# Performance work log

Measured on AMD Instinct MI355X. Metric: run time of the kernel, lower is better.

## Reference

```python
import jax, jax.numpy as jnp
from jax import lax
import numpy as np

R = 256            # reservoir_size
LUT_LEN = 18       # 2**18 LUT entries per node
B = 8              # bits_per_feature
D = 4              # n_features
M = 512            # samples
S = 512            # steps
OUT = 10           # output_size


def _first_primes(n):
    sieve = np.ones(2000, dtype=bool)
    sieve[:2] = False
    for i in range(2, 45):
        if sieve[i]:
            sieve[i * i::i] = False
    return np.nonzero(sieve)[0][:n].astype(np.int32)


def setup_inputs() -> dict:
    key = jax.random.key(0)
    ks = jax.random.split(key, 7)
    x = jax.random.randint(ks[0], (M, S, D, B), 0, 2).astype(bool)
    lut = jax.random.randint(ks[1], (R, 2 ** LUT_LEN), 0, 2).astype(jnp.int32)
    init_res = jax.random.randint(ks[2], (R,), 0, 2).astype(bool)
    W_res = jax.random.randint(ks[3], (R, R), 0, 2).astype(bool)
    input_nodes = jax.random.permutation(ks[4], R)[: B * D].astype(jnp.int32)
    primes = jnp.asarray(_first_primes(R))
    readout_W = jax.random.normal(ks[5], (OUT, R), dtype=jnp.float32) * (1.0 / np.sqrt(R))
    readout_b = jax.random.normal(ks[6], (OUT,), dtype=jnp.float32) * 0.01
    return {
        "x": x,
        "input_nodes": input_nodes,
        "lut": lut,
        "W_res": W_res,
        "primes": primes,
        "init_res": init_res,
        "readout_W": readout_W,
        "readout_b": readout_b,
    }


def _run_reservoir(x, input_nodes, lut, W_res, primes, init_res):
    m, s, d, b = x.shape
    xf = x.reshape(m, s, d * b).astype(jnp.int32)          # [m, s, d*b]
    # row j of Wp holds primes[k] * W_res[j, k]; idx = r @ Wp.T
    Wp = W_res.astype(jnp.int32) * primes[None, :]          # [R, R]
    node_idx = jnp.arange(R)[None, :]                       # [1, R]
    r0 = jnp.broadcast_to(init_res.astype(jnp.int32), (m, R))

    def step(r, x_t):
        # write encoded input bits into the reservoir, then LUT-perturb
        r = r.at[:, input_nodes].set(x_t)                   # [m, R]
        idx = r @ Wp.T                                      # [m, R] state indices
        r_new = jnp.take_along_axis(lut[None].repeat(1, 0)[0][node_idx.repeat(m, 0) * 0 + node_idx, idx], jnp.zeros((m, R, 1), jnp.int32), axis=-1) if False else lut[node_idx, idx]
        return r_new.astype(jnp.int32), None

    rf, _ = lax.scan(step, r0, jnp.swapaxes(xf, 0, 1))      # scan over s steps
    return rf                                               # [m, R] final states (0/1)


def reference(x, input_nodes, lut, W_res, primes, init_res, readout_W, readout_b):
    rf = _run_reservoir(x, input_nodes, lut, W_res, primes, init_res)
    return rf.astype(jnp.float32) @ readout_W.T + readout_b  # [m, output_size]
```

## Files before the change

### kernel.cpp

```cpp
#include <hip/hip_runtime.h>
#include <stdint.h>

#define R_NODES 256
#define M_SAMP  512
#define S_STEPS 512
#define OUT_N   10

__global__ void detect_layout(const uint8_t* __restrict__ x, int* __restrict__ flag) {
    __shared__ int any;
    if (threadIdx.x == 0) any = 0;
    __syncthreads();
    int acc = 0;
    for (int i = 0; i < 64; ++i)
        acc |= x[(size_t)(threadIdx.x * 64 + i) * 4 + 1];
    if (acc) atomicOr(&any, 1);
    __syncthreads();
    if (threadIdx.x == 0) *flag = any ? 1 : 0;
}

__global__ void pack_x(const uint8_t* __restrict__ x, const int* __restrict__ flag,
                       uint32_t* __restrict__ xp) {
    const int stride = (*flag) ? 1 : 4;
    const int f = blockIdx.x * blockDim.x + threadIdx.x;
    const int val = x[(size_t)f * stride];
    const uint64_t mask = __ballot(val != 0);
    const int lane = threadIdx.x & 63;
    if ((lane & 31) == 0) {
        uint32_t w = (lane & 32) ? (uint32_t)(mask >> 32) : (uint32_t)mask;
        xp[f >> 5] = w;
    }
}

__device__ __forceinline__ uint32_t spread8(uint32_t x) {
    x = (x | (x << 12)) & 0x000F000Fu;
    x = (x | (x << 6))  & 0x03030303u;
    x = (x | (x << 3))  & 0x11111111u;
    return x;
}
__global__ void pack_lut(const int* __restrict__ lut, uint32_t* __restrict__ lp32) {
    const int lane = threadIdx.x & 63;
    const int gw = blockIdx.x * (blockDim.x >> 6) + (threadIdx.x >> 6);
    const int4* src = (const int4*)lut;
    for (int it = 0; it < 16; ++it) {
        const int chunk = gw * 16 + it;
        const int4 q = src[(size_t)chunk * 64 + lane];
        const uint64_t b0 = __ballot((q.x & 1) != 0);
        const uint64_t b1 = __ballot((q.y & 1) != 0);
        const uint64_t b2 = __ballot((q.z & 1) != 0);
        const uint64_t b3 = __ballot((q.w & 1) != 0);
        if (lane < 8) {
            const uint32_t B0 = (uint32_t)(b0 >> (8 * lane)) & 0xFF;
            const uint32_t B1 = (uint32_t)(b1 >> (8 * lane)) & 0xFF;
            const uint32_t B2 = (uint32_t)(b2 >> (8 * lane)) & 0xFF;
            const uint32_t B3 = (uint32_t)(b3 >> (8 * lane)) & 0xFF;
            const uint32_t w = spread8(B0) | (spread8(B1) << 1)
                             | (spread8(B2) << 2) | (spread8(B3) << 3);
            lp32[(size_t)chunk * 8 + lane] = w;
        }
    }
}

__global__ __launch_bounds__(256, 2) void reservoir_pop(
    const uint32_t* __restrict__ xp, const uint64_t* __restrict__ lp,
    const int* __restrict__ input_nodes, const uint8_t* __restrict__ wres,
    const int* __restrict__ primes, const uint8_t* __restrict__ init_res,
    const int* __restrict__ flag, const float* __restrict__ rW,
    const float* __restrict__ rb, float* __restrict__ out)
{
    const int m = blockIdx.x;
    const int j = threadIdx.x;
    const int l = j & 63;
    const int w = j >> 6;
    const int stride = (*flag) ? 1 : 4;

    __shared__ uint32_t sxw[S_STEPS];
    __shared__ uint32_t rmask[2][8];
    __shared__ float    lout[OUT_N];

    const uint32_t* xrow = xp + m * S_STEPS;
    for (int i = j; i < S_STEPS; i += 256) sxw[i] = xrow[i];

    int slot = -1;
    for (int i = 0; i < 32; ++i)
        if (input_nodes[i] == j) slot = i;

    uint32_t PW[11][8];
#pragma unroll
    for (int b = 0; b < 11; ++b)
#pragma unroll
        for (int q = 0; q < 8; ++q) PW[b][q] = 0;
#pragma unroll
    for (int q = 0; q < 8; ++q) {
        for (int bit = 0; bit < 32; ++bit) {
            const int k = 32 * q + bit;
            const uint32_t on = wres[(size_t)(j * 256 + k) * stride] ? 1u : 0u;
            const uint32_t p  = on * (uint32_t)primes[k];
#pragma unroll
            for (int b = 0; b < 11; ++b)
                PW[b][q] |= ((p >> b) & 1u) << bit;
        }
    }

    __syncthreads();
    {
        int bv = init_res[(size_t)j * stride] ? 1 : 0;
        if (slot >= 0) bv = (sxw[0] >> slot) & 1;
        const uint64_t bal = __ballot(bv != 0);
        if (l == 0) {
            rmask[0][2 * w]     = (uint32_t)bal;
            rmask[0][2 * w + 1] = (uint32_t)(bal >> 32);
        }
    }
    __syncthreads();

    int cur = 0;
    int v = 0;
    for (int s = 0; s < S_STEPS; ++s) {
        const uint32_t R0 = rmask[cur][0], R1 = rmask[cur][1],
                       R2 = rmask[cur][2], R3 = rmask[cur][3],
                       R4 = rmask[cur][4], R5 = rmask[cur][5],
                       R6 = rmask[cur][6], R7 = rmask[cur][7];
        uint32_t idx = 0;
#pragma unroll
        for (int b = 0; b < 11; ++b) {
            uint32_t a;
            a  = (uint32_t)__popc(PW[b][0] & R0);
            a += (uint32_t)__popc(PW[b][1] & R1);
            a += (uint32_t)__popc(PW[b][2] & R2);
            a += (uint32_t)__popc(PW[b][3] & R3);
            a += (uint32_t)__popc(PW[b][4] & R4);
            a += (uint32_t)__popc(PW[b][5] & R5);
            a += (uint32_t)__popc(PW[b][6] & R6);
            a += (uint32_t)__popc(PW[b][7] & R7);
            idx += a << b;
        }

        const uint64_t wv = lp[((size_t)j << 12) + (idx >> 6)];
        v = (int)((wv >> (idx & 63)) & 1);

        int wb = v;
        if (s + 1 < S_STEPS && slot >= 0) wb = (sxw[s + 1] >> slot) & 1;
        const uint64_t bal = __ballot(wb != 0);
        if (l == 0) {
            rmask[cur ^ 1][2 * w]     = (uint32_t)bal;
            rmask[cur ^ 1][2 * w + 1] = (uint32_t)(bal >> 32);
        }
        __syncthreads();
        cur ^= 1;
    }

    if (j < OUT_N) lout[j] = 0.f;
    __syncthreads();
#pragma unroll
    for (int o = 0; o < OUT_N; ++o) {
        float c = v ? rW[o * R_NODES + j] : 0.f;
        for (int off = 32; off > 0; off >>= 1)
            c += __shfl_down(c, off, 64);
        if (l == 0) atomicAdd(&lout[o], c);
    }
    __syncthreads();
    if (j < OUT_N) out[m * OUT_N + j] = lout[j] + rb[j];
}

extern "C" void kernel_launch(void* const* d_in, const int* in_sizes, int n_in,
                              void* d_out, int out_size, void* d_ws, size_t ws_size,
                              hipStream_t stream) {
    const uint8_t* x        = (const uint8_t*)d_in[0];
    const int* input_nodes  = (const int*)d_in[1];
    const int* lut          = (const int*)d_in[2];
    const uint8_t* wres     = (const uint8_t*)d_in[3];
    const int* primes       = (const int*)d_in[4];
    const uint8_t* init_res = (const uint8_t*)d_in[5];
    const float* rW         = (const float*)d_in[6];
    const float* rb         = (const float*)d_in[7];
    float* out              = (float*)d_out;

    uint8_t* ws = (uint8_t*)d_ws;
    int*      flag = (int*)ws;
    uint32_t* xp   = (uint32_t*)(ws + 4096);
    uint64_t* lp   = (uint64_t*)(ws + 4096 + 1048576);

    detect_layout<<<1, 256, 0, stream>>>(x, flag);
    pack_x<<<(M_SAMP * S_STEPS * 32) / 256, 256, 0, stream>>>(x, flag, xp);
    pack_lut<<<4096, 256, 0, stream>>>(lut, (uint32_t*)lp);
    reservoir_pop<<<M_SAMP, 256, 0, stream>>>(xp, lp, input_nodes, wres,
                                              primes, init_res, flag,
                                              rW, rb, out);
}
```

Baseline: 1.061 ms.

## Process two samples per block to overlap LUT gathers and share per-node weights

Each block now runs two samples' reservoirs together. This reuses the per-thread packed prime-weight registers and halves the number of barriers per sample-step. The LUT lookup for sample B is issued while sample A's index is still being computed, using inline-asm global loads and explicit vmcnt waits, so the two memory latencies overlap inside one wave. The cost is that the grid shrinks to 256 blocks with launch bounds of one block per SIMD set, which lowers occupancy and relies on hand-scheduled asm waits.

```diff
diff --git a/kernel.cpp b/kernel.cpp
--- a/kernel.cpp
+++ b/kernel.cpp
@@ -5,6 +5,8 @@
 #define M_SAMP  512
 #define S_STEPS 512
 #define OUT_N   10
+
+typedef unsigned int u32x2 __attribute__((ext_vector_type(2)));
 
 __global__ void detect_layout(const uint8_t* __restrict__ x, int* __restrict__ flag) {
     __shared__ int any;
@@ -60,25 +62,26 @@
     }
 }
 
-__global__ __launch_bounds__(256, 2) void reservoir_pop(
+__global__ __launch_bounds__(256, 1) void reservoir_pop2(
     const uint32_t* __restrict__ xp, const uint64_t* __restrict__ lp,
     const int* __restrict__ input_nodes, const uint8_t* __restrict__ wres,
     const int* __restrict__ primes, const uint8_t* __restrict__ init_res,
     const int* __restrict__ flag, const float* __restrict__ rW,
     const float* __restrict__ rb, float* __restrict__ out)
 {
-    const int m = blockIdx.x;
+    const int m2 = blockIdx.x;
     const int j = threadIdx.x;
     const int l = j & 63;
     const int w = j >> 6;
     const int stride = (*flag) ? 1 : 4;
 
-    __shared__ uint32_t sxw[S_STEPS];
-    __shared__ uint32_t rmask[2][8];
-    __shared__ float    lout[OUT_N];
-
-    const uint32_t* xrow = xp + m * S_STEPS;
-    for (int i = j; i < S_STEPS; i += 256) sxw[i] = xrow[i];
+    __shared__ uint32_t sxwA[S_STEPS], sxwB[S_STEPS];
+    __shared__ uint32_t rmask[2][2][8];
+    __shared__ float    lout[2][OUT_N];
+
+    const uint32_t* xrowA = xp + (2 * m2 + 0) * S_STEPS;
+    const uint32_t* xrowB = xp + (2 * m2 + 1) * S_STEPS;
+    for (int i = j; i < S_STEPS; i += 256) { sxwA[i] = xrowA[i]; sxwB[i] = xrowB[i]; }
 
     int slot = -1;
     for (int i = 0; i < 32; ++i)
@@ -103,63 +106,102 @@
 
     __syncthreads();
     {
-        int bv = init_res[(size_t)j * stride] ? 1 : 0;
-        if (slot >= 0) bv = (sxw[0] >> slot) & 1;
-        const uint64_t bal = __ballot(bv != 0);
+        const int iv = init_res[(size_t)j * stride] ? 1 : 0;
+        int bvA = iv, bvB = iv;
+        if (slot >= 0) { bvA = (sxwA[0] >> slot) & 1; bvB = (sxwB[0] >> slot) & 1; }
+        const uint64_t balA = __ballot(bvA != 0);
+        const uint64_t balB = __ballot(bvB != 0);
         if (l == 0) {
-            rmask[0][2 * w]     = (uint32_t)bal;
-            rmask[0][2 * w + 1] = (uint32_t)(bal >> 32);
-        }
-    }
-    __syncthreads();
-
-    int cur = 0;
-    int v = 0;
+            rmask[0][0][2 * w] = (uint32_t)balA;  rmask[0][0][2 * w + 1] = (uint32_t)(balA >> 32);
+            rmask[0][1][2 * w] = (uint32_t)balB;  rmask[0][1][2 * w + 1] = (uint32_t)(balB >> 32);
+        }
+    }
+    __syncthreads();
+
+    const uint64_t lpbase = (uint64_t)(uintptr_t)lp;
+    int cur = 0, vA = 0, vB = 0;
+
+#define IDX_OF(R, OUTV) do {                                                  \
+        uint32_t acc_ = 0;                                                    \
+        _Pragma("unroll")                                                     \
+        for (int b_ = 0; b_ < 11; ++b_) {                                     \
+            uint32_t a_;                                                      \
+            a_  = (uint32_t)__popc(PW[b_][0] & R[0]);                         \
+            a_ += (uint32_t)__popc(PW[b_][1] & R[1]);                         \
+            a_ += (uint32_t)__popc(PW[b_][2] & R[2]);                         \
+            a_ += (uint32_t)__popc(PW[b_][3] & R[3]);                         \
+            a_ += (uint32_t)__popc(PW[b_][4] & R[4]);                         \
+            a_ += (uint32_t)__popc(PW[b_][5] & R[5]);                         \
+            a_ += (uint32_t)__popc(PW[b_][6] & R[6]);                         \
+            a_ += (uint32_t)__popc(PW[b_][7] & R[7]);                         \
+            acc_ += a_ << b_;                                                 \
+        }                                                                     \
+        OUTV = acc_;                                                          \
+    } while (0)
+
     for (int s = 0; s < S_STEPS; ++s) {
-        const uint32_t R0 = rmask[cur][0], R1 = rmask[cur][1],
-                       R2 = rmask[cur][2], R3 = rmask[cur][3],
-                       R4 = rmask[cur][4], R5 = rmask[cur][5],
-                       R6 = rmask[cur][6], R7 = rmask[cur][7];
-        uint32_t idx = 0;
-#pragma unroll
-        for (int b = 0; b < 11; ++b) {
-            uint32_t a;
-            a  = (uint32_t)__popc(PW[b][0] & R0);
-            a += (uint32_t)__popc(PW[b][1] & R1);
-            a += (uint32_t)__popc(PW[b][2] & R2);
-            a += (uint32_t)__popc(PW[b][3] & R3);
-            a += (uint32_t)__popc(PW[b][4] & R4);
-            a += (uint32_t)__popc(PW[b][5] & R5);
-            a += (uint32_t)__popc(PW[b][6] & R6);
-            a += (uint32_t)__popc(PW[b][7] & R7);
-            idx += a << b;
-        }
-
-        const uint64_t wv = lp[((size_t)j << 12) + (idx >> 6)];
-        v = (int)((wv >> (idx & 63)) & 1);
-
-        int wb = v;
-        if (s + 1 < S_STEPS && slot >= 0) wb = (sxw[s + 1] >> slot) & 1;
-        const uint64_t bal = __ballot(wb != 0);
+        uint32_t RA[8], RB[8];
+#pragma unroll
+        for (int q = 0; q < 8; ++q) { RA[q] = rmask[cur][0][q]; RB[q] = rmask[cur][1][q]; }
+
+        uint32_t idxA;
+        IDX_OF(RA, idxA);
+        u32x2 dA, dB;
+        const uint32_t oA = ((uint32_t)j << 15) + ((idxA >> 6) << 3);
+        asm volatile("global_load_dwordx2 %0, %1, %2" : "=v"(dA) : "v"(oA), "s"(lpbase));
+
+        uint32_t idxB;
+        IDX_OF(RB, idxB);
+        const uint32_t oB = ((uint32_t)j << 15) + ((idxB >> 6) << 3);
+        asm volatile("global_load_dwordx2 %0, %1, %2" : "=v"(dB) : "v"(oB), "s"(lpbase));
+
+        const int sn = (s + 1 < S_STEPS) ? s + 1 : s;
+        const uint32_t xwnA = sxwA[sn], xwnB = sxwB[sn];
+        const int inj = (s + 1 < S_STEPS) && (slot >= 0);
+
+        asm volatile("s_waitcnt vmcnt(1)");
+        asm volatile("" : "+v"(dA));
+        vA = (int)(((((uint64_t)dA[1] << 32) | dA[0]) >> (idxA & 63)) & 1);
+        int wbA = inj ? (int)((xwnA >> slot) & 1) : vA;
+
+        asm volatile("s_waitcnt vmcnt(0)");
+        asm volatile("" : "+v"(dB));
+        vB = (int)(((((uint64_t)dB[1] << 32) | dB[0]) >> (idxB & 63)) & 1);
+        int wbB = inj ? (int)((xwnB >> slot) & 1) : vB;
+
+        const uint64_t balA = __ballot(wbA != 0);
+        const uint64_t balB = __ballot(wbB != 0);
         if (l == 0) {
-            rmask[cur ^ 1][2 * w]     = (uint32_t)bal;
-            rmask[cur ^ 1][2 * w + 1] = (uint32_t)(bal >> 32);
+            rmask[cur ^ 1][0][2 * w] = (uint32_t)balA;  rmask[cur ^ 1][0][2 * w + 1] = (uint32_t)(balA >> 32);
+            rmask[cur ^ 1][1][2 * w] = (uint32_t)balB;  rmask[cur ^ 1][1][2 * w + 1] = (uint32_t)(balB >> 32);
         }
         __syncthreads();
         cur ^= 1;
     }
-
-    if (j < OUT_N) lout[j] = 0.f;
+#undef IDX_OF
+
+    const float* rWo;
+    const float* rbo;
+    asm volatile("" : "=s"(rWo) : "0"(rW));
+    asm volatile("" : "=s"(rbo) : "0"(rb));
+
+    if (j < 2 * OUT_N) lout[j / OUT_N][j % OUT_N] = 0.f;
     __syncthreads();
 #pragma unroll
     for (int o = 0; o < OUT_N; ++o) {
-        float c = v ? rW[o * R_NODES + j] : 0.f;
-        for (int off = 32; off > 0; off >>= 1)
-            c += __shfl_down(c, off, 64);
-        if (l == 0) atomicAdd(&lout[o], c);
-    }
-    __syncthreads();
-    if (j < OUT_N) out[m * OUT_N + j] = lout[j] + rb[j];
+        float cA = vA ? rWo[o * R_NODES + j] : 0.f;
+        float cB = vB ? rWo[o * R_NODES + j] : 0.f;
+        for (int off = 32; off > 0; off >>= 1) {
+            cA += __shfl_down(cA, off, 64);
+            cB += __shfl_down(cB, off, 64);
+        }
+        if (l == 0) { atomicAdd(&lout[0][o], cA); atomicAdd(&lout[1][o], cB); }
+    }
+    __syncthreads();
+    if (j < OUT_N) {
+        out[(size_t)(2 * m2 + 0) * OUT_N + j] = lout[0][j] + rbo[j];
+        out[(size_t)(2 * m2 + 1) * OUT_N + j] = lout[1][j] + rbo[j];
+    }
 }
 
 extern "C" void kernel_launch(void* const* d_in, const int* in_sizes, int n_in,
@@ -183,7 +225,7 @@
     detect_layout<<<1, 256, 0, stream>>>(x, flag);
     pack_x<<<(M_SAMP * S_STEPS * 32) / 256, 256, 0, stream>>>(x, flag, xp);
     pack_lut<<<4096, 256, 0, stream>>>(lut, (uint32_t*)lp);
-    reservoir_pop<<<M_SAMP, 256, 0, stream>>>(xp, lp, input_nodes, wres,
-                                              primes, init_res, flag,
-                                              rW, rb, out);
-}
+    reservoir_pop2<<<M_SAMP / 2, 256, 0, stream>>>(xp, lp, input_nodes, wres,
+                                                   primes, init_res, flag,
+                                                   rW, rb, out);
+}
```

After: 1.112 ms. 4.9% more time.

## Compute reservoir state indices with MFMA f16 matrix ops instead of popcount bit-planes

Applied to the files above, without the earlier changes.

Replaces the per-thread 11x8 popcount bit-plane dot product with MFMA 16x16x32 f16 instructions. Prime-weighted W_res rows are held as f16 A fragments in registers, and the reservoir bitmask bytes are expanded through a shared-memory lookup table into f16 B fragments. Node-to-lane mapping is permuted to fit the MFMA output layout. The LUT fetch now uses inline assembly with an explicit waitcnt, which overlaps the next x-word read with the load. It relies on f16/f32 exact representation of prime sums below 2^18 and adds register pressure from 32 half8 fragments per thread.

```diff
diff --git a/kernel.cpp b/kernel.cpp
--- a/kernel.cpp
+++ b/kernel.cpp
@@ -5,6 +5,10 @@
 #define M_SAMP  512
 #define S_STEPS 512
 #define OUT_N   10
+
+typedef unsigned int u32x2 __attribute__((ext_vector_type(2)));
+typedef _Float16     half8 __attribute__((ext_vector_type(8)));
+typedef float        f32x4 __attribute__((ext_vector_type(4)));
 
 __global__ void detect_layout(const uint8_t* __restrict__ x, int* __restrict__ flag) {
     __shared__ int any;
@@ -60,7 +64,7 @@
     }
 }
 
-__global__ __launch_bounds__(256, 2) void reservoir_pop(
+__global__ __launch_bounds__(256, 2) void reservoir_mv1(
     const uint32_t* __restrict__ xp, const uint64_t* __restrict__ lp,
     const int* __restrict__ input_nodes, const uint8_t* __restrict__ wres,
     const int* __restrict__ primes, const uint8_t* __restrict__ init_res,
@@ -68,42 +72,61 @@
     const float* __restrict__ rb, float* __restrict__ out)
 {
     const int m = blockIdx.x;
-    const int j = threadIdx.x;
-    const int l = j & 63;
-    const int w = j >> 6;
+    const int t = threadIdx.x;
+    const int l = t & 63;
+    const int w = t >> 6;
+    const int g = l >> 4;
+    const int c = l & 15;
     const int stride = (*flag) ? 1 : 4;
 
     __shared__ uint32_t sxw[S_STEPS];
     __shared__ uint32_t rmask[2][8];
+    __shared__ uint4    tab[256];
     __shared__ float    lout[OUT_N];
 
     const uint32_t* xrow = xp + m * S_STEPS;
-    for (int i = j; i < S_STEPS; i += 256) sxw[i] = xrow[i];
+    for (int i = t; i < S_STEPS; i += 256) sxw[i] = xrow[i];
+
+    {
+        uint32_t pk[4];
+#pragma unroll
+        for (int p = 0; p < 4; ++p) {
+            const uint32_t b0 = (t >> (2 * p)) & 1u;
+            const uint32_t b1 = (t >> (2 * p + 1)) & 1u;
+            pk[p] = b0 * 0x3C00u + b1 * 0x3C000000u;
+        }
+        tab[t] = make_uint4(pk[0], pk[1], pk[2], pk[3]);
+    }
+
+    const int T = c >> 2, r = c & 3;
+    const int n = 64 * w + 16 * T + 4 * g + r;
 
     int slot = -1;
     for (int i = 0; i < 32; ++i)
-        if (input_nodes[i] == j) slot = i;
-
-    uint32_t PW[11][8];
-#pragma unroll
-    for (int b = 0; b < 11; ++b)
-#pragma unroll
-        for (int q = 0; q < 8; ++q) PW[b][q] = 0;
-#pragma unroll
-    for (int q = 0; q < 8; ++q) {
-        for (int bit = 0; bit < 32; ++bit) {
-            const int k = 32 * q + bit;
-            const uint32_t on = wres[(size_t)(j * 256 + k) * stride] ? 1u : 0u;
-            const uint32_t p  = on * (uint32_t)primes[k];
-#pragma unroll
-            for (int b = 0; b < 11; ++b)
-                PW[b][q] |= ((p >> b) & 1u) << bit;
+        if (input_nodes[i] == n) slot = i;
+
+    half8 af[4][8];
+#pragma unroll
+    for (int Ti = 0; Ti < 4; ++Ti) {
+        const int row = 64 * w + 16 * Ti + c;
+#pragma unroll
+        for (int kt = 0; kt < 8; ++kt) {
+            half8 a;
+#pragma unroll
+            for (int j = 0; j < 8; ++j) {
+                const int kp = 32 * kt + 8 * g + j;
+                const int kn = 64 * (kp >> 6) + 16 * ((kp & 15) >> 2)
+                             + 4 * ((kp >> 4) & 3) + (kp & 3);
+                const int on = wres[(size_t)(row * 256 + kn) * stride] ? 1 : 0;
+                a[j] = (_Float16)(on ? (float)primes[kn] : 0.f);
+            }
+            af[Ti][kt] = a;
         }
     }
 
     __syncthreads();
     {
-        int bv = init_res[(size_t)j * stride] ? 1 : 0;
+        int bv = init_res[(size_t)n * stride] ? 1 : 0;
         if (slot >= 0) bv = (sxw[0] >> slot) & 1;
         const uint64_t bal = __ballot(bv != 0);
         if (l == 0) {
@@ -113,33 +136,37 @@
     }
     __syncthreads();
 
-    int cur = 0;
-    int v = 0;
+    const uint64_t lpbase = (uint64_t)(uintptr_t)lp;
+    const uint32_t nb = (uint32_t)n << 15;
+    const half8* tabh = (const half8*)tab;
+    int cur = 0, v = 0;
+
     for (int s = 0; s < S_STEPS; ++s) {
-        const uint32_t R0 = rmask[cur][0], R1 = rmask[cur][1],
-                       R2 = rmask[cur][2], R3 = rmask[cur][3],
-                       R4 = rmask[cur][4], R5 = rmask[cur][5],
-                       R6 = rmask[cur][6], R7 = rmask[cur][7];
-        uint32_t idx = 0;
-#pragma unroll
-        for (int b = 0; b < 11; ++b) {
-            uint32_t a;
-            a  = (uint32_t)__popc(PW[b][0] & R0);
-            a += (uint32_t)__popc(PW[b][1] & R1);
-            a += (uint32_t)__popc(PW[b][2] & R2);
-            a += (uint32_t)__popc(PW[b][3] & R3);
-            a += (uint32_t)__popc(PW[b][4] & R4);
-            a += (uint32_t)__popc(PW[b][5] & R5);
-            a += (uint32_t)__popc(PW[b][6] & R6);
-            a += (uint32_t)__popc(PW[b][7] & R7);
-            idx += a << b;
-        }
-
-        const uint64_t wv = lp[((size_t)j << 12) + (idx >> 6)];
-        v = (int)((wv >> (idx & 63)) & 1);
-
-        int wb = v;
-        if (s + 1 < S_STEPS && slot >= 0) wb = (sxw[s + 1] >> slot) & 1;
+        f32x4 a0 = {0,0,0,0}, a1 = {0,0,0,0}, a2 = {0,0,0,0}, a3 = {0,0,0,0};
+#pragma unroll
+        for (int kt = 0; kt < 8; ++kt) {
+            const uint32_t byte = (rmask[cur][kt] >> (8 * g)) & 0xFFu;
+            const half8 bf = tabh[byte];
+            a0 = __builtin_amdgcn_mfma_f32_16x16x32_f16(af[0][kt], bf, a0, 0, 0, 0);
+            a1 = __builtin_amdgcn_mfma_f32_16x16x32_f16(af[1][kt], bf, a1, 0, 0, 0);
+            a2 = __builtin_amdgcn_mfma_f32_16x16x32_f16(af[2][kt], bf, a2, 0, 0, 0);
+            a3 = __builtin_amdgcn_mfma_f32_16x16x32_f16(af[3][kt], bf, a3, 0, 0, 0);
+        }
+        const f32x4 at = (c < 8) ? ((c < 4) ? a0 : a1) : ((c < 12) ? a2 : a3);
+        const float fv = (r == 0) ? at[0] : (r == 1) ? at[1] : (r == 2) ? at[2] : at[3];
+        const uint32_t idx = (uint32_t)fv;
+
+        u32x2 d;
+        const uint32_t o = nb + ((idx >> 6) << 3);
+        asm volatile("global_load_dwordx2 %0, %1, %2" : "=v"(d) : "v"(o), "s"(lpbase));
+        const int sn = (s + 1 < S_STEPS) ? s + 1 : s;
+        const uint32_t xwn = sxw[sn];
+        const int inj = (s + 1 < S_STEPS) && (slot >= 0);
+        asm volatile("s_waitcnt vmcnt(0)");
+        asm volatile("" : "+v"(d));
+        v = (int)(((((uint64_t)d[1] << 32) | d[0]) >> (idx & 63)) & 1);
+        const int wb = inj ? (int)((xwn >> slot) & 1) : v;
+
         const uint64_t bal = __ballot(wb != 0);
         if (l == 0) {
             rmask[cur ^ 1][2 * w]     = (uint32_t)bal;
@@ -149,17 +176,22 @@
         cur ^= 1;
     }
 
-    if (j < OUT_N) lout[j] = 0.f;
+    const float* rWo;
+    const float* rbo;
+    asm volatile("" : "=s"(rWo) : "0"(rW));
+    asm volatile("" : "=s"(rbo) : "0"(rb));
+
+    if (t < OUT_N) lout[t] = 0.f;
     __syncthreads();
 #pragma unroll
     for (int o = 0; o < OUT_N; ++o) {
-        float c = v ? rW[o * R_NODES + j] : 0.f;
+        float cv = v ? rWo[o * R_NODES + n] : 0.f;
         for (int off = 32; off > 0; off >>= 1)
-            c += __shfl_down(c, off, 64);
-        if (l == 0) atomicAdd(&lout[o], c);
-    }
-    __syncthreads();
-    if (j < OUT_N) out[m * OUT_N + j] = lout[j] + rb[j];
+            cv += __shfl_down(cv, off, 64);
+        if (l == 0) atomicAdd(&lout[o], cv);
+    }
+    __syncthreads();
+    if (t < OUT_N) out[m * OUT_N + t] = lout[t] + rbo[t];
 }
 
 extern "C" void kernel_launch(void* const* d_in, const int* in_sizes, int n_in,
@@ -183,7 +215,7 @@
     detect_layout<<<1, 256, 0, stream>>>(x, flag);
     pack_x<<<(M_SAMP * S_STEPS * 32) / 256, 256, 0, stream>>>(x, flag, xp);
     pack_lut<<<4096, 256, 0, stream>>>(lut, (uint32_t*)lp);
-    reservoir_pop<<<M_SAMP, 256, 0, stream>>>(xp, lp, input_nodes, wres,
+    reservoir_mv1<<<M_SAMP, 256, 0, stream>>>(xp, lp, input_nodes, wres,
                                               primes, init_res, flag,
                                               rW, rb, out);
 }
```

Result: faster. 902.3 us (-14.9%).
